# Kernel tuning notes

Measured on AMD Instinct MI355X. Metric: run time of the kernel, lower is better.

The kernel has to match this reference:

```python
import jax, jax.numpy as jnp
import numpy as np

N_USERS = 100000
N_ITEMS = 50000
N_NODES = N_USERS + N_ITEMS
EMBED_DIM = 64
N_LAYERS = 3
NNZ = 2400000
BATCH = 16384


def setup_inputs() -> dict:
    key = jax.random.key(0)
    ks = jax.random.split(key, 8)
    user_embed_weight = jax.random.normal(ks[0], (N_USERS, EMBED_DIM), dtype=jnp.float32) * 0.1
    item_embed_weight = jax.random.normal(ks[1], (N_ITEMS, EMBED_DIM), dtype=jnp.float32) * 0.1
    adj_row = jax.random.randint(ks[2], (NNZ,), 0, N_NODES, dtype=jnp.int32)
    adj_col = jax.random.randint(ks[3], (NNZ,), 0, N_NODES, dtype=jnp.int32)
    # positive normalized-ish edge weights (stand-in for D^-1/2 A D^-1/2 values)
    adj_vals = jax.random.uniform(ks[4], (NNZ,), dtype=jnp.float32) * 0.1
    users = jax.random.randint(ks[5], (BATCH,), 0, N_USERS, dtype=jnp.int32)
    pos_items = jax.random.randint(ks[6], (BATCH,), 0, N_ITEMS, dtype=jnp.int32)
    neg_items = jax.random.randint(ks[7], (BATCH,), 0, N_ITEMS, dtype=jnp.int32)
    return {
        "user_embed_weight": user_embed_weight,
        "item_embed_weight": item_embed_weight,
        "adj_vals": adj_vals,
        "adj_row": adj_row,
        "adj_col": adj_col,
        "users": users,
        "pos_items": pos_items,
        "neg_items": neg_items,
    }


def _spmm(vals, row, col, x, n):
    # sparse [n,n] @ dense [n,d] via gather + segment-sum
    return jax.ops.segment_sum(vals[:, None] * x[col], row, num_segments=n)


def reference(user_embed_weight, item_embed_weight, adj_vals, adj_row, adj_col,
              users, pos_items, neg_items):
    n = user_embed_weight.shape[0] + item_embed_weight.shape[0]
    all_embed = jnp.concatenate([user_embed_weight, item_embed_weight], axis=0)
    acc = all_embed
    x = all_embed
    for _ in range(N_LAYERS):
        x = _spmm(adj_vals, adj_row, adj_col, x, n)
        acc = acc + x
    final_embed = acc / (N_LAYERS + 1)
    user_emb = final_embed[: user_embed_weight.shape[0]]
    item_emb = final_embed[user_embed_weight.shape[0]:]

    u = user_emb[users]
    p = item_emb[pos_items]
    nn_ = item_emb[neg_items]
    pos_score = jnp.sum(u * p, axis=1)
    neg_score = jnp.sum(u * nn_, axis=1)
    loss = -jnp.mean(jnp.log(jax.nn.sigmoid(pos_score - neg_score) + 1e-08))
    reg_loss = (jnp.sum(user_embed_weight[users] ** 2)
                + jnp.sum(item_embed_weight[pos_items] ** 2)
                + jnp.sum(item_embed_weight[neg_items] ** 2)) / users.shape[0]
    return (loss, reg_loss)
```

## Files before the change

### kernel.cpp

```cpp
#include <hip/hip_runtime.h>

#define N_USERS 100000
#define N_ITEMS 50000
#define N_NODES (N_USERS + N_ITEMS)
#define DIM 64
#define BATCH 16384
#define RPB 512
#define BSHIFT 9
#define NB ((N_NODES + RPB - 1) / RPB)
#define HP 296
#define EPT 8
#define TILE_E (512 * EPT)
#define STRIDE 12288
#define XSCALE 64.0f
#define INV_XSCALE 0.015625f
#define SB ((N_NODES + 15) / 16)
#define WLB ((3 * BATCH) / 16)

struct __align__(8) Pair { int c; float v; };
typedef float floatx2 __attribute__((ext_vector_type(2)));

__device__ __forceinline__ unsigned pk8(float a, float b, float c, float d) {
    int w = __builtin_amdgcn_cvt_pk_fp8_f32(a, b, 0, false);
    w = __builtin_amdgcn_cvt_pk_fp8_f32(c, d, w, true);
    return (unsigned)w;
}

#define EDGE_F8D(V, X) { \
    floatx2 lo_ = __builtin_amdgcn_cvt_pk_f32_fp8((X), false); \
    floatx2 hi_ = __builtin_amdgcn_cvt_pk_f32_fp8((X), true); \
    a0 = fmaf((V), lo_.x, a0); a1 = fmaf((V), lo_.y, a1); \
    a2 = fmaf((V), hi_.x, a2); a3 = fmaf((V), hi_.y, a3); }

__device__ __forceinline__ float block_reduce_sum(float v) {
    for (int s = 32; s > 0; s >>= 1) v += __shfl_xor(v, s, 64);
    __shared__ float sm[8];
    int lane = threadIdx.x & 63;
    int wid  = threadIdx.x >> 6;
    if (lane == 0) sm[wid] = v;
    __syncthreads();
    float t = 0.0f;
    if (threadIdx.x == 0) {
        int nw = (blockDim.x + 63) >> 6;
        for (int w = 0; w < nw; ++w) t += sm[w];
    }
    return t;
}

__global__ void convert_kernel(const float* __restrict__ uw, const float* __restrict__ iw,
                               unsigned char* __restrict__ x8,
                               int* __restrict__ flags, int* __restrict__ bcursor,
                               float* __restrict__ sums, int* __restrict__ ctrl) {
    size_t tid = (size_t)blockIdx.x * 256 + threadIdx.x;
    if (tid == 0) { sums[0] = 0.0f; sums[1] = 0.0f; ctrl[0] = 0; ctrl[1] = 0; }
    if (tid < N_NODES) flags[tid] = 0;
    else if (tid < N_NODES + NB) bcursor[tid - N_NODES] = 0;
    size_t base = tid * 8;
    if (base >= (size_t)N_NODES * DIM) return;
    const float* src = (base < (size_t)N_USERS * DIM) ? uw + base
                                                      : iw + (base - (size_t)N_USERS * DIM);
    float4 a = ((const float4*)src)[0];
    float4 b = ((const float4*)src)[1];
    uint2 o;
    o.x = pk8(XSCALE * a.x, XSCALE * a.y, XSCALE * a.z, XSCALE * a.w);
    o.y = pk8(XSCALE * b.x, XSCALE * b.y, XSCALE * b.z, XSCALE * b.w);
    *(uint2*)(x8 + base) = o;
}

template<bool DOWL>
__global__ void init_kernel(const float* __restrict__ uw, const float* __restrict__ iw,
                            const int* __restrict__ users, const int* __restrict__ pos,
                            const int* __restrict__ neg,
                            float* __restrict__ uacc, float* __restrict__ pacc,
                            float* __restrict__ nacc, float* __restrict__ reg_sum,
                            int* __restrict__ flags, int* __restrict__ wl,
                            int* __restrict__ ctrl) {
    int tid = blockIdx.x * blockDim.x + threadIdx.x;
    if (DOWL && tid < 3 * BATCH) {
        int r = (tid < BATCH) ? users[tid]
              : (tid < 2 * BATCH) ? N_USERS + pos[tid - BATCH]
              : N_USERS + neg[tid - 2 * BATCH];
        if (atomicExch(&flags[r], 1) == 0) wl[atomicAdd(&ctrl[0], 1)] = r;
    }
    int i = tid >> 4;
    int q = tid & 15;
    if (i >= BATCH) return;
    size_t o = (size_t)i * DIM + q * 4;
    float4 u = *(const float4*)(uw + (size_t)users[i] * DIM + q * 4);
    float4 p = *(const float4*)(iw + (size_t)pos[i]   * DIM + q * 4);
    float4 n = *(const float4*)(iw + (size_t)neg[i]   * DIM + q * 4);
    *(float4*)(uacc + o) = u;
    *(float4*)(pacc + o) = p;
    *(float4*)(nacc + o) = n;
    float ss = u.x*u.x + u.y*u.y + u.z*u.z + u.w*u.w
             + p.x*p.x + p.y*p.y + p.z*p.z + p.w*p.w
             + n.x*n.x + n.y*n.y + n.z*n.z + n.w*n.w;
    float bt = block_reduce_sum(ss);
    if (threadIdx.x == 0) unsafeAtomicAdd(reg_sum, bt);
}

__global__ void binned_scatter_kernel(const int* __restrict__ rows, const int* __restrict__ cols,
                                      const float* __restrict__ vals, int* __restrict__ bcursor,
                                      Pair* __restrict__ bcv, int nnz) {
    __shared__ int h[8][HP];
    int t = threadIdx.x, w = t >> 6;
    for (int i = t; i < 8 * HP; i += 512) ((int*)h)[i] = 0;
    __syncthreads();
    long long tile = (long long)blockIdx.x * TILE_E;
    int er[EPT], cr[EPT];
    float vr[EPT];
    #pragma unroll
    for (int j = 0; j < EPT; ++j) {
        long long e = tile + t + j * 512;
        if (e < nnz) {
            int r = rows[e];
            er[j] = r;
            cr[j] = cols[e];
            vr[j] = vals[e];
            atomicAdd(&h[w][r >> BSHIFT], 1);
        } else er[j] = -1;
    }
    __syncthreads();
    for (int b = t; b < NB; b += 512) {
        int cw[8], tot = 0;
        #pragma unroll
        for (int w2 = 0; w2 < 8; ++w2) { cw[w2] = h[w2][b]; tot += cw[w2]; }
        int base = tot ? (b * STRIDE + atomicAdd(&bcursor[b], tot)) : 0;
        #pragma unroll
        for (int w2 = 0; w2 < 8; ++w2) { h[w2][b] = base; base += cw[w2]; }
    }
    __syncthreads();
    #pragma unroll
    for (int j = 0; j < EPT; ++j) {
        if (er[j] >= 0) {
            int r = er[j];
            int dst = atomicAdd(&h[w][r >> BSHIFT], 1);
            Pair p;
            p.c = cr[j] | ((r & (RPB - 1)) << 18);
            p.v = vr[j];
            bcv[dst] = p;
        }
    }
}

__global__ void post_scan_kernel(const int* __restrict__ counts, int* __restrict__ bbase,
                                 int* __restrict__ rowptr, int nnz) {
    __shared__ int sm[512];
    int t = threadIdx.x;
    int v = (t < NB) ? counts[t] : 0;
    sm[t] = v;
    __syncthreads();
    for (int off = 1; off < 512; off <<= 1) {
        int tmp = (t >= off) ? sm[t - off] : 0;
        __syncthreads();
        sm[t] += tmp;
        __syncthreads();
    }
    if (t < NB) bbase[t] = sm[t] - v;
    if (t == 511) bbase[NB] = sm[511];
    if (t == 0) rowptr[N_NODES] = nnz;
}

__global__ void bucket_sort_kernel(const Pair* __restrict__ bcv,
                                   const int* __restrict__ counts,
                                   const int* __restrict__ bbase,
                                   int* __restrict__ rowptr, Pair* __restrict__ perm) {
    __shared__ int rh8[8][RPB + 8];
    __shared__ int rh[RPB];
    __shared__ int sc[RPB];
    int blk = blockIdx.x;
    int t = threadIdx.x;
    int w = t >> 6;
    size_t src = (size_t)blk * STRIDE;
    int base = bbase[blk];
    int cnt  = counts[blk];
    for (int i = t; i < 8 * (RPB + 8); i += 512) ((int*)rh8)[i] = 0;
    __syncthreads();
    for (int i = t; i < cnt; i += 512)
        atomicAdd(&rh8[w][(unsigned)bcv[src + i].c >> 18], 1);
    __syncthreads();
    int v = 0;
    #pragma unroll
    for (int w2 = 0; w2 < 8; ++w2) v += rh8[w2][t];
    sc[t] = v;
    __syncthreads();
    for (int off = 1; off < 512; off <<= 1) {
        int tmp = (t >= off) ? sc[t - off] : 0;
        __syncthreads();
        sc[t] += tmp;
        __syncthreads();
    }
    int excl = sc[t] - v;
    int g = blk * RPB + t;
    if (g < N_NODES) rowptr[g] = base + excl;
    rh[t] = excl;
    __syncthreads();
    for (int i = t; i < cnt; i += 512) {
        Pair p = bcv[src + i];
        int r = (unsigned)p.c >> 18;
        int rk = atomicAdd(&rh[r], 1);
        p.c &= 0x3FFFF;
        perm[base + rk] = p;
    }
}

__device__ __forceinline__ void spmm_row_f8(const unsigned char* __restrict__ x8,
                                            const Pair* __restrict__ pe,
                                            int e, int end, int q, int row,
                                            unsigned char* __restrict__ out8) {
    float a0 = 0.f, a1 = 0.f, a2 = 0.f, a3 = 0.f;
    for (; e + 7 < end; e += 8) {
        Pair p0 = pe[e],     p1 = pe[e + 1], p2 = pe[e + 2], p3 = pe[e + 3];
        Pair p4 = pe[e + 4], p5 = pe[e + 5], p6 = pe[e + 6], p7 = pe[e + 7];
        unsigned x0 = *(const unsigned*)(x8 + ((size_t)p0.c << 6) + q * 4);
        unsigned x1 = *(const unsigned*)(x8 + ((size_t)p1.c << 6) + q * 4);
        unsigned x2 = *(const unsigned*)(x8 + ((size_t)p2.c << 6) + q * 4);
        unsigned x3 = *(const unsigned*)(x8 + ((size_t)p3.c << 6) + q * 4);
        unsigned x4 = *(const unsigned*)(x8 + ((size_t)p4.c << 6) + q * 4);
        unsigned x5 = *(const unsigned*)(x8 + ((size_t)p5.c << 6) + q * 4);
        unsigned x6 = *(const unsigned*)(x8 + ((size_t)p6.c << 6) + q * 4);
        unsigned x7 = *(const unsigned*)(x8 + ((size_t)p7.c << 6) + q * 4);
        EDGE_F8D(p0.v, x0); EDGE_F8D(p1.v, x1);
        EDGE_F8D(p2.v, x2); EDGE_F8D(p3.v, x3);
        EDGE_F8D(p4.v, x4); EDGE_F8D(p5.v, x5);
        EDGE_F8D(p6.v, x6); EDGE_F8D(p7.v, x7);
    }
    for (; e + 1 < end; e += 2) {
        Pair p0 = pe[e], p1 = pe[e + 1];
        unsigned x0 = *(const unsigned*)(x8 + ((size_t)p0.c << 6) + q * 4);
        unsigned x1 = *(const unsigned*)(x8 + ((size_t)p1.c << 6) + q * 4);
        EDGE_F8D(p0.v, x0); EDGE_F8D(p1.v, x1);
    }
    if (e < end) {
        Pair p = pe[e];
        unsigned x = *(const unsigned*)(x8 + ((size_t)p.c << 6) + q * 4);
        EDGE_F8D(p.v, x);
    }
    *(unsigned*)(out8 + ((size_t)row << 6) + q * 4) = pk8(a0, a1, a2, a3);
}

__global__ void spmm_f8_kernel(const unsigned char* __restrict__ x8,
                               const Pair* __restrict__ pe,
                               const int* __restrict__ rowptr,
                               unsigned char* __restrict__ out8) {
    int row = blockIdx.x * 16 + (threadIdx.x >> 4);
    if (row >= N_NODES) return;
    spmm_row_f8(x8, pe, rowptr[row], rowptr[row + 1], threadIdx.x & 15, row, out8);
}

__global__ void spmm_wl_f8_kernel(const unsigned char* __restrict__ x8,
                                  const Pair* __restrict__ pe,
                                  const int* __restrict__ rowptr,
                                  const int* __restrict__ wl,
                                  const int* __restrict__ ctrl,
                                  unsigned char* __restrict__ out8) {
    int idx = blockIdx.x * 16 + (threadIdx.x >> 4);
    if (idx >= ctrl[0]) return;
    int row = wl[idx];
    spmm_row_f8(x8, pe, rowptr[row], rowptr[row + 1], threadIdx.x & 15, row, out8);
}

__global__ void spmm_atomic_kernel(const float* __restrict__ xu, const float* __restrict__ xi,
                                   const float* __restrict__ vals, const int* __restrict__ rows,
                                   const int* __restrict__ cols,
                                   float* __restrict__ out, int nnz) {
    long long tid = (long long)blockIdx.x * blockDim.x + threadIdx.x;
    int e = (int)(tid >> 4);
    if (e >= nnz) return;
    int q = (int)(tid & 15);
    int r = rows[e];
    int c = cols[e];
    float v = vals[e];
    const float* src = (c < N_USERS) ? (xu + (size_t)c * DIM)
                                     : (xi + (size_t)(c - N_USERS) * DIM);
    float4 x = *(const float4*)(src + q * 4);
    float* dst = out + (size_t)r * DIM + q * 4;
    unsafeAtomicAdd(dst + 0, v * x.x);
    unsafeAtomicAdd(dst + 1, v * x.y);
    unsafeAtomicAdd(dst + 2, v * x.z);
    unsafeAtomicAdd(dst + 3, v * x.w);
}

__global__ void gather_add_f8_kernel(const unsigned char* __restrict__ x8,
                                     const int* __restrict__ users, const int* __restrict__ pos,
                                     const int* __restrict__ neg,
                                     float* __restrict__ uacc, float* __restrict__ pacc,
                                     float* __restrict__ nacc) {
    int tid = blockIdx.x * blockDim.x + threadIdx.x;
    int i = tid >> 4;
    int q = tid & 15;
    if (i >= BATCH) return;
    size_t o = (size_t)i * DIM + q * 4;
    float4 a;
    unsigned u;
    floatx2 lo, hi;

    a = *(float4*)(uacc + o);
    u = *(const unsigned*)(x8 + ((size_t)users[i] << 6) + q * 4);
    lo = __builtin_amdgcn_cvt_pk_f32_fp8(u, false);
    hi = __builtin_amdgcn_cvt_pk_f32_fp8(u, true);
    a.x = fmaf(lo.x, INV_XSCALE, a.x); a.y = fmaf(lo.y, INV_XSCALE, a.y);
    a.z = fmaf(hi.x, INV_XSCALE, a.z); a.w = fmaf(hi.y, INV_XSCALE, a.w);
    *(float4*)(uacc + o) = a;

    a = *(float4*)(pacc + o);
    u = *(const unsigned*)(x8 + ((size_t)(N_USERS + pos[i]) << 6) + q * 4);
    lo = __builtin_amdgcn_cvt_pk_f32_fp8(u, false);
    hi = __builtin_amdgcn_cvt_pk_f32_fp8(u, true);
    a.x = fmaf(lo.x, INV_XSCALE, a.x); a.y = fmaf(lo.y, INV_XSCALE, a.y);
    a.z = fmaf(hi.x, INV_XSCALE, a.z); a.w = fmaf(hi.y, INV_XSCALE, a.w);
    *(float4*)(pacc + o) = a;

    a = *(float4*)(nacc + o);
    u = *(const unsigned*)(x8 + ((size_t)(N_USERS + neg[i]) << 6) + q * 4);
    lo = __builtin_amdgcn_cvt_pk_f32_fp8(u, false);
    hi = __builtin_amdgcn_cvt_pk_f32_fp8(u, true);
    a.x = fmaf(lo.x, INV_XSCALE, a.x); a.y = fmaf(lo.y, INV_XSCALE, a.y);
    a.z = fmaf(hi.x, INV_XSCALE, a.z); a.w = fmaf(hi.y, INV_XSCALE, a.w);
    *(float4*)(nacc + o) = a;
}

__global__ void gather_score_kernel(const unsigned char* __restrict__ x8,
                                    const int* __restrict__ users, const int* __restrict__ pos,
                                    const int* __restrict__ neg,
                                    const float* __restrict__ uacc, const float* __restrict__ pacc,
                                    const float* __restrict__ nacc, float* __restrict__ sums,
                                    int* __restrict__ ctrl, float* __restrict__ out) {
    int tid = blockIdx.x * blockDim.x + threadIdx.x;
    int i = tid >> 4;
    int q = tid & 15;
    float ps = 0.0f, ns = 0.0f;
    if (i < BATCH) {
        size_t o = (size_t)i * DIM + q * 4;
        float4 u = *(const float4*)(uacc + o);
        float4 p = *(const float4*)(pacc + o);
        float4 n = *(const float4*)(nacc + o);
        unsigned t;
        floatx2 lo, hi;
        t = *(const unsigned*)(x8 + ((size_t)users[i] << 6) + q * 4);
        lo = __builtin_amdgcn_cvt_pk_f32_fp8(t, false);
        hi = __builtin_amdgcn_cvt_pk_f32_fp8(t, true);
        u.x = fmaf(lo.x, INV_XSCALE, u.x); u.y = fmaf(lo.y, INV_XSCALE, u.y);
        u.z = fmaf(hi.x, INV_XSCALE, u.z); u.w = fmaf(hi.y, INV_XSCALE, u.w);
        t = *(const unsigned*)(x8 + ((size_t)(N_USERS + pos[i]) << 6) + q * 4);
        lo = __builtin_amdgcn_cvt_pk_f32_fp8(t, false);
        hi = __builtin_amdgcn_cvt_pk_f32_fp8(t, true);
        p.x = fmaf(lo.x, INV_XSCALE, p.x); p.y = fmaf(lo.y, INV_XSCALE, p.y);
        p.z = fmaf(hi.x, INV_XSCALE, p.z); p.w = fmaf(hi.y, INV_XSCALE, p.w);
        t = *(const unsigned*)(x8 + ((size_t)(N_USERS + neg[i]) << 6) + q * 4);
        lo = __builtin_amdgcn_cvt_pk_f32_fp8(t, false);
        hi = __builtin_amdgcn_cvt_pk_f32_fp8(t, true);
        n.x = fmaf(lo.x, INV_XSCALE, n.x); n.y = fmaf(lo.y, INV_XSCALE, n.y);
        n.z = fmaf(hi.x, INV_XSCALE, n.z); n.w = fmaf(hi.y, INV_XSCALE, n.w);
        ps = u.x*p.x + u.y*p.y + u.z*p.z + u.w*p.w;
        ns = u.x*n.x + u.y*n.y + u.z*n.z + u.w*n.w;
    }
    for (int s = 8; s > 0; s >>= 1) {
        ps += __shfl_xor(ps, s, 16);
        ns += __shfl_xor(ns, s, 16);
    }
    float term = 0.0f;
    if (q == 0 && i < BATCH) {
        float d = (ps - ns) * (1.0f / 16.0f);
        float sig = 1.0f / (1.0f + expf(-d));
        term = logf(sig + 1e-8f);
    }
    float bt = block_reduce_sum(term);
    if (threadIdx.x == 0) {
        unsafeAtomicAdd(&sums[0], bt);
        __threadfence();
        int tk = atomicAdd(&ctrl[1], 1);
        if (tk == (int)gridDim.x - 1) {
            float ls = unsafeAtomicAdd(&sums[0], 0.0f);
            float rs = unsafeAtomicAdd(&sums[1], 0.0f);
            out[0] = -ls / (float)BATCH;
            out[1] =  rs / (float)BATCH;
        }
    }
}

__global__ void gather_add_kernel(const float* __restrict__ x,
                                  const int* __restrict__ users, const int* __restrict__ pos,
                                  const int* __restrict__ neg,
                                  float* __restrict__ uacc, float* __restrict__ pacc,
                                  float* __restrict__ nacc) {
    int tid = blockIdx.x * blockDim.x + threadIdx.x;
    int i = tid >> 4;
    int q = tid & 15;
    if (i >= BATCH) return;
    size_t o = (size_t)i * DIM + q * 4;
    float4 a, b;
    a = *(float4*)(uacc + o);
    b = *(const float4*)(x + (size_t)users[i] * DIM + q * 4);
    a.x += b.x; a.y += b.y; a.z += b.z; a.w += b.w;
    *(float4*)(uacc + o) = a;
    a = *(float4*)(pacc + o);
    b = *(const float4*)(x + (size_t)(N_USERS + pos[i]) * DIM + q * 4);
    a.x += b.x; a.y += b.y; a.z += b.z; a.w += b.w;
    *(float4*)(pacc + o) = a;
    a = *(float4*)(nacc + o);
    b = *(const float4*)(x + (size_t)(N_USERS + neg[i]) * DIM + q * 4);
    a.x += b.x; a.y += b.y; a.z += b.z; a.w += b.w;
    *(float4*)(nacc + o) = a;
}

__global__ void score_kernel(const float* __restrict__ uacc, const float* __restrict__ pacc,
                             const float* __restrict__ nacc, float* __restrict__ loss_sum) {
    int tid = blockIdx.x * blockDim.x + threadIdx.x;
    int i = tid >> 4;
    int q = tid & 15;
    float ps = 0.0f, ns = 0.0f;
    if (i < BATCH) {
        size_t o = (size_t)i * DIM + q * 4;
        float4 u = *(const float4*)(uacc + o);
        float4 p = *(const float4*)(pacc + o);
        float4 n = *(const float4*)(nacc + o);
        ps = u.x*p.x + u.y*p.y + u.z*p.z + u.w*p.w;
        ns = u.x*n.x + u.y*n.y + u.z*n.z + u.w*n.w;
    }
    for (int s = 8; s > 0; s >>= 1) {
        ps += __shfl_xor(ps, s, 16);
        ns += __shfl_xor(ns, s, 16);
    }
    float term = 0.0f;
    if (q == 0 && i < BATCH) {
        float d = (ps - ns) * (1.0f / 16.0f);
        float sig = 1.0f / (1.0f + expf(-d));
        term = logf(sig + 1e-8f);
    }
    float bt = block_reduce_sum(term);
    if (threadIdx.x == 0) unsafeAtomicAdd(loss_sum, bt);
}

__global__ void finalize_kernel(const float* __restrict__ sums, float* __restrict__ out) {
    if (threadIdx.x == 0 && blockIdx.x == 0) {
        out[0] = -sums[0] / (float)BATCH;
        out[1] =  sums[1] / (float)BATCH;
    }
}

static inline size_t align256(size_t x) { return (x + 255) & ~(size_t)255; }

extern "C" void kernel_launch(void* const* d_in, const int* in_sizes, int n_in,
                              void* d_out, int out_size, void* d_ws, size_t ws_size,
                              hipStream_t stream) {
    const float* uw   = (const float*)d_in[0];
    const float* iw   = (const float*)d_in[1];
    const float* vals = (const float*)d_in[2];
    const int*   rows = (const int*)d_in[3];
    const int*   cols = (const int*)d_in[4];
    const int*   users = (const int*)d_in[5];
    const int*   pos   = (const int*)d_in[6];
    const int*   neg   = (const int*)d_in[7];
    const int nnz = in_sizes[2];

    char* ws = (char*)d_ws;
    const size_t nodeBytes = (size_t)N_NODES * DIM * sizeof(float);
    const size_t qBytes    = (size_t)N_NODES * DIM;
    const size_t accBytes  = (size_t)BATCH * DIM * sizeof(float);

    size_t off = 0;
    char*  nodeReg = ws + off;            off += align256(2 * nodeBytes);
    float* uacc = (float*)(ws + off);     off += align256(accBytes);
    float* pacc = (float*)(ws + off);     off += align256(accBytes);
    float* nacc = (float*)(ws + off);     off += align256(accBytes);
    float* sums = (float*)(ws + off);     off += 256;
    int*   ctrl = (int*)(ws + off);       off += 256;
    Pair*  perm = (Pair*)(ws + off);      off += align256((size_t)nnz * sizeof(Pair));
    int*   rowptr = (int*)(ws + off);     off += align256((size_t)(N_NODES + 1) * sizeof(int));
    int*   bbase  = (int*)(ws + off);     off += align256((size_t)(NB + 1) * sizeof(int));
    int*   bcursor= (int*)(ws + off);     off += align256((size_t)NB * sizeof(int));
    int*   flags  = (int*)(ws + off);     off += align256((size_t)N_NODES * sizeof(int));
    int*   wl     = (int*)(ws + off);     off += align256((size_t)(3 * BATCH) * sizeof(int));
    const bool fits_alias = (2 * align256(qBytes) + (size_t)NB * STRIDE * sizeof(Pair)) <= 2 * nodeBytes;
    const bool use_csr = (off <= ws_size) && fits_alias && (N_NODES < (1 << 18));

    unsigned char* xb0 = (unsigned char*)nodeReg;
    unsigned char* xb1 = (unsigned char*)(nodeReg + align256(qBytes));
    unsigned char* xb2 = (unsigned char*)(nodeReg + 2 * align256(qBytes));
    Pair*          bcv = (Pair*)(nodeReg + 2 * align256(qBytes));
    float* xA = (float*)nodeReg;
    float* xB = (float*)(nodeReg + nodeBytes);

    float* out = (float*)d_out;

    const int bthreads = BATCH * 16;
    const int bblocks  = bthreads / 256;
    const int tblocks  = (nnz + TILE_E - 1) / TILE_E;
    const int cblocks  = (int)(((size_t)N_NODES * DIM / 8 + 255) / 256);

    if (use_csr) {
        convert_kernel<<<cblocks, 256, 0, stream>>>(uw, iw, xb0, flags, bcursor, sums, ctrl);
        init_kernel<true><<<bblocks, 256, 0, stream>>>(uw, iw, users, pos, neg,
                                                       uacc, pacc, nacc, sums + 1, flags, wl, ctrl);
        binned_scatter_kernel<<<tblocks, 512, 0, stream>>>(rows, cols, vals, bcursor, bcv, nnz);
        post_scan_kernel<<<1, 512, 0, stream>>>(bcursor, bbase, rowptr, nnz);
        bucket_sort_kernel<<<NB, 512, 0, stream>>>(bcv, bcursor, bbase, rowptr, perm);

        spmm_f8_kernel<<<SB, 256, 0, stream>>>(xb0, perm, rowptr, xb1);
        gather_add_f8_kernel<<<bblocks, 256, 0, stream>>>(xb1, users, pos, neg, uacc, pacc, nacc);
        spmm_f8_kernel<<<SB, 256, 0, stream>>>(xb1, perm, rowptr, xb2);
        gather_add_f8_kernel<<<bblocks, 256, 0, stream>>>(xb2, users, pos, neg, uacc, pacc, nacc);
        spmm_wl_f8_kernel<<<WLB, 256, 0, stream>>>(xb2, perm, rowptr, wl, ctrl, xb0);
        gather_score_kernel<<<bblocks, 256, 0, stream>>>(xb0, users, pos, neg,
                                                         uacc, pacc, nacc, sums, ctrl, out);
    } else {
        const long long sthreads = (long long)nnz * 16;
        const int sblocks = (int)((sthreads + 255) / 256);
        (void)hipMemsetAsync(sums, 0, 2 * sizeof(float), stream);
        (void)hipMemsetAsync(ctrl, 0, 2 * sizeof(int), stream);
        init_kernel<false><<<bblocks, 256, 0, stream>>>(uw, iw, users, pos, neg,
                                                        uacc, pacc, nacc, sums + 1, flags, wl, ctrl);
        (void)hipMemsetAsync(xA, 0, nodeBytes, stream);
        spmm_atomic_kernel<<<sblocks, 256, 0, stream>>>(uw, iw, vals, rows, cols, xA, nnz);
        gather_add_kernel<<<bblocks, 256, 0, stream>>>(xA, users, pos, neg, uacc, pacc, nacc);
        (void)hipMemsetAsync(xB, 0, nodeBytes, stream);
        spmm_atomic_kernel<<<sblocks, 256, 0, stream>>>(xA, xA + (size_t)N_USERS * DIM, vals, rows, cols, xB, nnz);
        gather_add_kernel<<<bblocks, 256, 0, stream>>>(xB, users, pos, neg, uacc, pacc, nacc);
        (void)hipMemsetAsync(xA, 0, nodeBytes, stream);
        spmm_atomic_kernel<<<sblocks, 256, 0, stream>>>(xB, xB + (size_t)N_USERS * DIM, vals, rows, cols, xA, nnz);
        gather_add_kernel<<<bblocks, 256, 0, stream>>>(xA, users, pos, neg, uacc, pacc, nacc);
        score_kernel<<<bblocks, 256, 0, stream>>>(uacc, pacc, nacc, sums);
        finalize_kernel<<<1, 1, 0, stream>>>(sums, out);
    }
}
```

Baseline: 234.8 us.

## Fuse scatter, fp8 convert and batch init into one heterogeneous build kernel

New measurement: 231.8 us. Within noise of the previous version (-1.3%).

```diff
diff --git a/kernel.cpp b/kernel.cpp
--- a/kernel.cpp
+++ b/kernel.cpp
@@ -9,13 +9,15 @@
 #define BSHIFT 9
 #define NB ((N_NODES + RPB - 1) / RPB)
 #define HP 296
-#define EPT 8
+#define EPT 4
 #define TILE_E (512 * EPT)
 #define STRIDE 12288
 #define XSCALE 64.0f
 #define INV_XSCALE 0.015625f
 #define SB ((N_NODES + 15) / 16)
 #define WLB ((3 * BATCH) / 16)
+#define CVB (((size_t)N_NODES * DIM / 8 + 511) / 512)
+#define INB (BATCH * 16 / 512)
 
 struct __align__(8) Pair { int c; float v; };
 typedef float floatx2 __attribute__((ext_vector_type(2)));
@@ -47,99 +49,95 @@
     return t;
 }
 
-__global__ void convert_kernel(const float* __restrict__ uw, const float* __restrict__ iw,
-                               unsigned char* __restrict__ x8,
-                               int* __restrict__ flags, int* __restrict__ bcursor,
-                               float* __restrict__ sums, int* __restrict__ ctrl) {
-    size_t tid = (size_t)blockIdx.x * 256 + threadIdx.x;
-    if (tid == 0) { sums[0] = 0.0f; sums[1] = 0.0f; ctrl[0] = 0; ctrl[1] = 0; }
-    if (tid < N_NODES) flags[tid] = 0;
-    else if (tid < N_NODES + NB) bcursor[tid - N_NODES] = 0;
-    size_t base = tid * 8;
-    if (base >= (size_t)N_NODES * DIM) return;
-    const float* src = (base < (size_t)N_USERS * DIM) ? uw + base
-                                                      : iw + (base - (size_t)N_USERS * DIM);
-    float4 a = ((const float4*)src)[0];
-    float4 b = ((const float4*)src)[1];
-    uint2 o;
-    o.x = pk8(XSCALE * a.x, XSCALE * a.y, XSCALE * a.z, XSCALE * a.w);
-    o.y = pk8(XSCALE * b.x, XSCALE * b.y, XSCALE * b.z, XSCALE * b.w);
-    *(uint2*)(x8 + base) = o;
-}
-
-template<bool DOWL>
-__global__ void init_kernel(const float* __restrict__ uw, const float* __restrict__ iw,
-                            const int* __restrict__ users, const int* __restrict__ pos,
-                            const int* __restrict__ neg,
-                            float* __restrict__ uacc, float* __restrict__ pacc,
-                            float* __restrict__ nacc, float* __restrict__ reg_sum,
-                            int* __restrict__ flags, int* __restrict__ wl,
-                            int* __restrict__ ctrl) {
-    int tid = blockIdx.x * blockDim.x + threadIdx.x;
-    if (DOWL && tid < 3 * BATCH) {
-        int r = (tid < BATCH) ? users[tid]
-              : (tid < 2 * BATCH) ? N_USERS + pos[tid - BATCH]
-              : N_USERS + neg[tid - 2 * BATCH];
-        if (atomicExch(&flags[r], 1) == 0) wl[atomicAdd(&ctrl[0], 1)] = r;
-    }
-    int i = tid >> 4;
-    int q = tid & 15;
-    if (i >= BATCH) return;
-    size_t o = (size_t)i * DIM + q * 4;
-    float4 u = *(const float4*)(uw + (size_t)users[i] * DIM + q * 4);
-    float4 p = *(const float4*)(iw + (size_t)pos[i]   * DIM + q * 4);
-    float4 n = *(const float4*)(iw + (size_t)neg[i]   * DIM + q * 4);
-    *(float4*)(uacc + o) = u;
-    *(float4*)(pacc + o) = p;
-    *(float4*)(nacc + o) = n;
-    float ss = u.x*u.x + u.y*u.y + u.z*u.z + u.w*u.w
-             + p.x*p.x + p.y*p.y + p.z*p.z + p.w*p.w
-             + n.x*n.x + n.y*n.y + n.z*n.z + n.w*n.w;
-    float bt = block_reduce_sum(ss);
-    if (threadIdx.x == 0) unsafeAtomicAdd(reg_sum, bt);
-}
-
-__global__ void binned_scatter_kernel(const int* __restrict__ rows, const int* __restrict__ cols,
-                                      const float* __restrict__ vals, int* __restrict__ bcursor,
-                                      Pair* __restrict__ bcv, int nnz) {
+__global__ void build_kernel(const int* __restrict__ rows, const int* __restrict__ cols,
+                             const float* __restrict__ vals, int* __restrict__ bcursor,
+                             Pair* __restrict__ bcv, int nnz, int scb,
+                             const float* __restrict__ uw, const float* __restrict__ iw,
+                             unsigned char* __restrict__ x8,
+                             const int* __restrict__ users, const int* __restrict__ pos,
+                             const int* __restrict__ neg,
+                             float* __restrict__ uacc, float* __restrict__ pacc,
+                             float* __restrict__ nacc, float* __restrict__ reg_sum,
+                             int* __restrict__ flags, int* __restrict__ wl,
+                             int* __restrict__ ctrl) {
     __shared__ int h[8][HP];
-    int t = threadIdx.x, w = t >> 6;
-    for (int i = t; i < 8 * HP; i += 512) ((int*)h)[i] = 0;
-    __syncthreads();
-    long long tile = (long long)blockIdx.x * TILE_E;
-    int er[EPT], cr[EPT];
-    float vr[EPT];
-    #pragma unroll
-    for (int j = 0; j < EPT; ++j) {
-        long long e = tile + t + j * 512;
-        if (e < nnz) {
-            int r = rows[e];
-            er[j] = r;
-            cr[j] = cols[e];
-            vr[j] = vals[e];
-            atomicAdd(&h[w][r >> BSHIFT], 1);
-        } else er[j] = -1;
-    }
-    __syncthreads();
-    for (int b = t; b < NB; b += 512) {
-        int cw[8], tot = 0;
+    int t = threadIdx.x;
+    if ((int)blockIdx.x < scb) {
+        int w = t >> 6;
+        for (int i = t; i < 8 * HP; i += 512) ((int*)h)[i] = 0;
+        __syncthreads();
+        long long tile = (long long)blockIdx.x * TILE_E;
+        int er[EPT], cr[EPT];
+        float vr[EPT];
         #pragma unroll
-        for (int w2 = 0; w2 < 8; ++w2) { cw[w2] = h[w2][b]; tot += cw[w2]; }
-        int base = tot ? (b * STRIDE + atomicAdd(&bcursor[b], tot)) : 0;
+        for (int j = 0; j < EPT; ++j) {
+            long long e = tile + t + j * 512;
+            if (e < nnz) {
+                int r = rows[e];
+                er[j] = r;
+                cr[j] = cols[e];
+                vr[j] = vals[e];
+                atomicAdd(&h[w][r >> BSHIFT], 1);
+            } else er[j] = -1;
+        }
+        __syncthreads();
+        for (int b = t; b < NB; b += 512) {
+            int cw[8], tot = 0;
+            #pragma unroll
+            for (int w2 = 0; w2 < 8; ++w2) { cw[w2] = h[w2][b]; tot += cw[w2]; }
+            int base = tot ? (b * STRIDE + atomicAdd(&bcursor[b], tot)) : 0;
+            #pragma unroll
+            for (int w2 = 0; w2 < 8; ++w2) { h[w2][b] = base; base += cw[w2]; }
+        }
+        __syncthreads();
         #pragma unroll
-        for (int w2 = 0; w2 < 8; ++w2) { h[w2][b] = base; base += cw[w2]; }
-    }
-    __syncthreads();
-    #pragma unroll
-    for (int j = 0; j < EPT; ++j) {
-        if (er[j] >= 0) {
-            int r = er[j];
-            int dst = atomicAdd(&h[w][r >> BSHIFT], 1);
-            Pair p;
-            p.c = cr[j] | ((r & (RPB - 1)) << 18);
-            p.v = vr[j];
-            bcv[dst] = p;
+        for (int j = 0; j < EPT; ++j) {
+            if (er[j] >= 0) {
+                int r = er[j];
+                int dst = atomicAdd(&h[w][r >> BSHIFT], 1);
+                Pair p;
+                p.c = cr[j] | ((r & (RPB - 1)) << 18);
+                p.v = vr[j];
+                bcv[dst] = p;
+            }
         }
+    } else if (blockIdx.x < (unsigned)(scb + (int)CVB)) {
+        size_t tid = (size_t)(blockIdx.x - scb) * 512 + t;
+        size_t base = tid * 8;
+        if (base >= (size_t)N_NODES * DIM) return;
+        const float* src = (base < (size_t)N_USERS * DIM) ? uw + base
+                                                          : iw + (base - (size_t)N_USERS * DIM);
+        float4 a = ((const float4*)src)[0];
+        float4 b = ((const float4*)src)[1];
+        uint2 o;
+        o.x = pk8(XSCALE * a.x, XSCALE * a.y, XSCALE * a.z, XSCALE * a.w);
+        o.y = pk8(XSCALE * b.x, XSCALE * b.y, XSCALE * b.z, XSCALE * b.w);
+        *(uint2*)(x8 + base) = o;
+    } else {
+        int tid = (int)(blockIdx.x - scb - (int)CVB) * 512 + t;
+        if (tid < 3 * BATCH) {
+            int r = (tid < BATCH) ? users[tid]
+                  : (tid < 2 * BATCH) ? N_USERS + pos[tid - BATCH]
+                  : N_USERS + neg[tid - 2 * BATCH];
+            if (atomicExch(&flags[r], 1) == 0) wl[atomicAdd(&ctrl[0], 1)] = r;
+        }
+        int i = tid >> 4;
+        int q = tid & 15;
+        float ss = 0.0f;
+        if (i < BATCH) {
+            size_t o = (size_t)i * DIM + q * 4;
+            float4 u = *(const float4*)(uw + (size_t)users[i] * DIM + q * 4);
+            float4 p = *(const float4*)(iw + (size_t)pos[i]   * DIM + q * 4);
+            float4 n = *(const float4*)(iw + (size_t)neg[i]   * DIM + q * 4);
+            *(float4*)(uacc + o) = u;
+            *(float4*)(pacc + o) = p;
+            *(float4*)(nacc + o) = n;
+            ss = u.x*u.x + u.y*u.y + u.z*u.z + u.w*u.w
+               + p.x*p.x + p.y*p.y + p.z*p.z + p.w*p.w
+               + n.x*n.x + n.y*n.y + n.z*n.z + n.w*n.w;
+        }
+        float bt = block_reduce_sum(ss);
+        if (t == 0) unsafeAtomicAdd(reg_sum, bt);
     }
 }
 
@@ -379,6 +377,29 @@
     }
 }
 
+__global__ void init_f32_kernel(const float* __restrict__ uw, const float* __restrict__ iw,
+                                const int* __restrict__ users, const int* __restrict__ pos,
+                                const int* __restrict__ neg,
+                                float* __restrict__ uacc, float* __restrict__ pacc,
+                                float* __restrict__ nacc, float* __restrict__ reg_sum) {
+    int tid = blockIdx.x * blockDim.x + threadIdx.x;
+    int i = tid >> 4;
+    int q = tid & 15;
+    if (i >= BATCH) return;
+    size_t o = (size_t)i * DIM + q * 4;
+    float4 u = *(const float4*)(uw + (size_t)users[i] * DIM + q * 4);
+    float4 p = *(const float4*)(iw + (size_t)pos[i]   * DIM + q * 4);
+    float4 n = *(const float4*)(iw + (size_t)neg[i]   * DIM + q * 4);
+    *(float4*)(uacc + o) = u;
+    *(float4*)(pacc + o) = p;
+    *(float4*)(nacc + o) = n;
+    float ss = u.x*u.x + u.y*u.y + u.z*u.z + u.w*u.w
+             + p.x*p.x + p.y*p.y + p.z*p.z + p.w*p.w
+             + n.x*n.x + n.y*n.y + n.z*n.z + n.w*n.w;
+    float bt = block_reduce_sum(ss);
+    if (threadIdx.x == 0) unsafeAtomicAdd(reg_sum, bt);
+}
+
 __global__ void gather_add_kernel(const float* __restrict__ x,
                                   const int* __restrict__ users, const int* __restrict__ pos,
                                   const int* __restrict__ neg,
@@ -464,13 +485,15 @@
     float* uacc = (float*)(ws + off);     off += align256(accBytes);
     float* pacc = (float*)(ws + off);     off += align256(accBytes);
     float* nacc = (float*)(ws + off);     off += align256(accBytes);
+    size_t zero_base = off;
     float* sums = (float*)(ws + off);     off += 256;
     int*   ctrl = (int*)(ws + off);       off += 256;
+    int*   bcursor= (int*)(ws + off);     off += align256((size_t)NB * sizeof(int));
+    int*   flags  = (int*)(ws + off);     off += align256((size_t)N_NODES * sizeof(int));
+    size_t zero_bytes = off - zero_base;
     Pair*  perm = (Pair*)(ws + off);      off += align256((size_t)nnz * sizeof(Pair));
     int*   rowptr = (int*)(ws + off);     off += align256((size_t)(N_NODES + 1) * sizeof(int));
     int*   bbase  = (int*)(ws + off);     off += align256((size_t)(NB + 1) * sizeof(int));
-    int*   bcursor= (int*)(ws + off);     off += align256((size_t)NB * sizeof(int));
-    int*   flags  = (int*)(ws + off);     off += align256((size_t)N_NODES * sizeof(int));
     int*   wl     = (int*)(ws + off);     off += align256((size_t)(3 * BATCH) * sizeof(int));
     const bool fits_alias = (2 * align256(qBytes) + (size_t)NB * STRIDE * sizeof(Pair)) <= 2 * nodeBytes;
     const bool use_csr = (off <= ws_size) && fits_alias && (N_NODES < (1 << 18));
@@ -486,14 +509,14 @@
 
     const int bthreads = BATCH * 16;
     const int bblocks  = bthreads / 256;
-    const int tblocks  = (nnz + TILE_E - 1) / TILE_E;
-    const int cblocks  = (int)(((size_t)N_NODES * DIM / 8 + 255) / 256);
+    const int scb      = (nnz + TILE_E - 1) / TILE_E;
 
     if (use_csr) {
-        convert_kernel<<<cblocks, 256, 0, stream>>>(uw, iw, xb0, flags, bcursor, sums, ctrl);
-        init_kernel<true><<<bblocks, 256, 0, stream>>>(uw, iw, users, pos, neg,
-                                                       uacc, pacc, nacc, sums + 1, flags, wl, ctrl);
-        binned_scatter_kernel<<<tblocks, 512, 0, stream>>>(rows, cols, vals, bcursor, bcv, nnz);
+        (void)hipMemsetAsync(ws + zero_base, 0, zero_bytes, stream);
+        build_kernel<<<scb + (int)CVB + INB, 512, 0, stream>>>(
+            rows, cols, vals, bcursor, bcv, nnz, scb,
+            uw, iw, xb0, users, pos, neg,
+            uacc, pacc, nacc, sums + 1, flags, wl, ctrl);
         post_scan_kernel<<<1, 512, 0, stream>>>(bcursor, bbase, rowptr, nnz);
         bucket_sort_kernel<<<NB, 512, 0, stream>>>(bcv, bcursor, bbase, rowptr, perm);
 
@@ -508,9 +531,8 @@
         const long long sthreads = (long long)nnz * 16;
         const int sblocks = (int)((sthreads + 255) / 256);
         (void)hipMemsetAsync(sums, 0, 2 * sizeof(float), stream);
-        (void)hipMemsetAsync(ctrl, 0, 2 * sizeof(int), stream);
-        init_kernel<false><<<bblocks, 256, 0, stream>>>(uw, iw, users, pos, neg,
-                                                        uacc, pacc, nacc, sums + 1, flags, wl, ctrl);
+        init_f32_kernel<<<bblocks, 256, 0, stream>>>(uw, iw, users, pos, neg,
+                                                     uacc, pacc, nacc, sums + 1);
         (void)hipMemsetAsync(xA, 0, nodeBytes, stream);
         spmm_atomic_kernel<<<sblocks, 256, 0, stream>>>(uw, iw, vals, rows, cols, xA, nnz);
         gather_add_kernel<<<bblocks, 256, 0, stream>>>(xA, users, pos, neg, uacc, pacc, nacc);
```
